# Optimization experiments

Measured on AMD Instinct MI355X. Metric: run time of the kernel, lower is better.

The kernel has to match this reference:

```python
import jax, jax.numpy as jnp
import numpy as np

N_EXPERTS = 64
TOPK = 4
DIM = 2048
B_T = 8192


def setup_inputs() -> dict:
    key = jax.random.key(0)
    k1, k2 = jax.random.split(key)
    x = jax.random.normal(k1, (B_T, DIM), jnp.float32)
    W = jax.random.normal(k2, (N_EXPERTS, DIM), jnp.float32) * 0.02  # nn.Linear weight (out, in)
    router_bias = jnp.zeros((N_EXPERTS,), jnp.float32)  # registered buffer, init zeros
    return {"x": x, "W": W, "router_bias": router_bias, "token_capacity": 3072}


def _route(x, W, router_bias, token_capacity):
    """Faithful serial greedy capacity-aware routing.

    Replicates the torch nested loop (k-major, token-minor order):
      - per step, pick argmax over the token's (mutated) logits among experts
        with remaining capacity;
      - full experts whose logit exceeds the chosen one get permanently set
        to -inf in that token's logit row (exactly what the inner while-style
        loop does);
      - if no expert has capacity, selected stays -1, weight 0, and the whole
        row becomes -inf (torch sets the top expert to -inf n_experts times).
    """
    logits0 = x @ W.T + router_bias                       # (N, E)
    scores = jax.nn.softmax(logits0, axis=-1)             # (N, E)
    cap = token_capacity // TOPK                          # python int
    remaining0 = jnp.full((N_EXPERTS,), float(cap), jnp.float32)
    N = x.shape[0]
    NEG = jnp.float32(-jnp.inf)

    def step(carry, i):
        logits, remaining = carry
        b = i % N                                         # token index (k-major order)
        row = logits[b]                                   # (E,)
        masked = jnp.where(remaining > 0, row, NEG)
        chosen = jnp.argmax(masked)
        ok = remaining[chosen] > 0                        # False only if all experts full
        sel = jnp.where(ok, chosen, -1).astype(jnp.int32)
        w = jnp.where(ok, scores[b, chosen], jnp.float32(0.0))
        full = remaining <= 0
        cval = row[chosen]
        # full experts 'above' the chosen one were visited and zapped to -inf
        new_row = jnp.where(ok,
                            jnp.where(full & (row > cval), NEG, row),
                            jnp.full_like(row, NEG))
        logits = logits.at[b].set(new_row)
        remaining = remaining.at[chosen].add(jnp.where(ok, jnp.float32(-1.0), jnp.float32(0.0)))
        return (logits, remaining), (sel, w)

    (_, _), (sel_f, w_f) = jax.lax.scan(step, (logits0, remaining0),
                                        jnp.arange(TOPK * N))
    selected = sel_f.reshape(TOPK, N).T                   # (N, TOPK)
    weights = w_f.reshape(TOPK, N).T                      # (N, TOPK)
    weights = weights / (weights.sum(axis=-1, keepdims=True) + 1e-8)
    return selected, weights


def reference(x, W, router_bias, token_capacity):
    return _route(x, W, router_bias, token_capacity)
```

## Files before the change

kernel.cpp:

```cpp
#include <hip/hip_runtime.h>
#include <math.h>

#define N_TOK 8192
#define DIM   2048
#define NE    64
#define TOPK  4
#define THETA 2e-3f
#define TPB2  16
#define NBLK  (N_TOK / TPB2)
#define RSTR  260

typedef short bf16x8 __attribute__((ext_vector_type(8)));
typedef float f32x4  __attribute__((ext_vector_type(4)));

#define AS1 __attribute__((address_space(1)))
#define AS3 __attribute__((address_space(3)))

#define OFF_LOGITS 0
#define OFF_MAXV   (OFF_LOGITS + N_TOK * NE)
#define OFF_DENOM  (OFF_MAXV + N_TOK)
#define OFF_W1     (OFF_DENOM + N_TOK)
#define OFF_C1     (OFF_W1 + N_TOK)
#define OFF_NFLAG  (OFF_C1 + N_TOK)
#define OFF_FLAGL  (OFF_NFLAG + 64)
#define OFF_WH     (OFF_FLAGL + N_TOK)
#define OFF_WL     (OFF_WH + NE * DIM / 2)
#define OFF_WT     (OFF_WL + NE * DIM / 2)
#define OFF_WTMP   (OFF_WT + NE * DIM)

__device__ inline void cvt2(float a, float b, unsigned& hi, unsigned& lo) {
    const unsigned ua = __float_as_uint(a), ub = __float_as_uint(b);
    hi = __builtin_amdgcn_perm(ub, ua, 0x07060302u);
    const float ra = a - __uint_as_float(ua & 0xFFFF0000u);
    const float rb = b - __uint_as_float(ub & 0xFFFF0000u);
    lo = __builtin_amdgcn_perm(__float_as_uint(rb), __float_as_uint(ra), 0x07060302u);
}

union FragU { unsigned u[4]; bf16x8 v; uint4 q; };

__device__ inline void make_frags(const float4& p, const float4& q,
                                  bf16x8& hi, bf16x8& lo) {
    FragU H, L;
    cvt2(p.x, p.y, H.u[0], L.u[0]);
    cvt2(p.z, p.w, H.u[1], L.u[1]);
    cvt2(q.x, q.y, H.u[2], L.u[2]);
    cvt2(q.z, q.w, H.u[3], L.u[3]);
    hi = H.v; lo = L.v;
}

__global__ __launch_bounds__(256)
void k_wc(const float* __restrict__ W, unsigned short* __restrict__ wh2,
          unsigned short* __restrict__ wl2, float* __restrict__ wt,
          int* __restrict__ nflag) {
    const int t = blockIdx.x * 256 + threadIdx.x;
    if (t == 0) nflag[0] = 0;
    const int l  = t & 63;
    const int grp = t >> 6;
    const int nt = grp & 3;
    const int kc = grp >> 2;
    const int e  = nt * 16 + (l & 15);
    const int k0 = kc * 32 + (l >> 4) * 8;

    const float4 p = *reinterpret_cast<const float4*>(W + (size_t)e * DIM + k0);
    const float4 q = *reinterpret_cast<const float4*>(W + (size_t)e * DIM + k0 + 4);
    FragU H, L;
    cvt2(p.x, p.y, H.u[0], L.u[0]);
    cvt2(p.z, p.w, H.u[1], L.u[1]);
    cvt2(q.x, q.y, H.u[2], L.u[2]);
    cvt2(q.z, q.w, H.u[3], L.u[3]);
    const size_t off = (size_t)grp * 512 + l * 8;
    *reinterpret_cast<uint4*>(wh2 + off) = H.q;
    *reinterpret_cast<uint4*>(wl2 + off) = L.q;

    wt[(size_t)(k0 + 0) * NE + e] = p.x;
    wt[(size_t)(k0 + 1) * NE + e] = p.y;
    wt[(size_t)(k0 + 2) * NE + e] = p.z;
    wt[(size_t)(k0 + 3) * NE + e] = p.w;
    wt[(size_t)(k0 + 4) * NE + e] = q.x;
    wt[(size_t)(k0 + 5) * NE + e] = q.y;
    wt[(size_t)(k0 + 6) * NE + e] = q.z;
    wt[(size_t)(k0 + 7) * NE + e] = q.w;
}

__global__ __launch_bounds__(512, 4)
void k_main(const float* __restrict__ x, const unsigned short* __restrict__ wh2,
            const unsigned short* __restrict__ wl2, const float* __restrict__ bias,
            float* __restrict__ logits, float* __restrict__ maxv,
            float* __restrict__ denomv, float* __restrict__ w1f,
            int* __restrict__ c1, int* __restrict__ nflag, int* __restrict__ flagl) {
    __shared__ __align__(16) float xs[2][TPB2 * RSTR];
    __shared__ float red[8][TPB2][68];
    __shared__ float lbuf[TPB2][68];

    const int tid = threadIdx.x;
    const int w   = tid >> 6;
    const int l   = tid & 63;
    const int t0  = blockIdx.x * TPB2;
    const int m   = l & 15;
    const int g   = l >> 4;

    const float* xrow0 = x + (size_t)(t0 + 2 * w) * DIM + l * 4;
    const float* xrow1 = x + (size_t)(t0 + 2 * w + 1) * DIM + l * 4;
    AS3 float* lds0 = (AS3 float*)&xs[0][(2 * w) * RSTR];
    AS3 float* lds1 = (AS3 float*)&xs[0][(2 * w + 1) * RSTR];
    const int xs1off = TPB2 * RSTR;

    const unsigned short* bh = wh2 + (size_t)w * 2048 + l * 8;
    const unsigned short* bl = wl2 + (size_t)w * 2048 + l * 8;

    f32x4 accA[4], accB[4];
    #pragma unroll
    for (int nt = 0; nt < 4; ++nt)
        #pragma unroll
        for (int r = 0; r < 4; ++r) { accA[nt][r] = 0.0f; accB[nt][r] = 0.0f; }

    __builtin_amdgcn_global_load_lds((const AS1 void*)xrow0, (AS3 void*)lds0, 16, 0, 0);
    __builtin_amdgcn_global_load_lds((const AS1 void*)xrow1, (AS3 void*)lds1, 16, 0, 0);
    uint4 BH[2][4], BL[2][4];
    #pragma unroll
    for (int nt = 0; nt < 4; ++nt) {
        BH[0][nt] = *reinterpret_cast<const uint4*>(bh + nt * 512);
        BL[0][nt] = *reinterpret_cast<const uint4*>(bl + nt * 512);
    }
    __syncthreads();

    const int aoff = m * RSTR + w * 32 + g * 8;

    #pragma unroll
    for (int win = 0; win < 8; ++win) {
        const int cur = win & 1, nxt = cur ^ 1;
        if (win < 7) {
            __builtin_amdgcn_global_load_lds(
                (const AS1 void*)(xrow0 + (win + 1) * 256),
                (AS3 void*)(lds0 + nxt * xs1off), 16, 0, 0);
            __builtin_amdgcn_global_load_lds(
                (const AS1 void*)(xrow1 + (win + 1) * 256),
                (AS3 void*)(lds1 + nxt * xs1off), 16, 0, 0);
            #pragma unroll
            for (int nt = 0; nt < 4; ++nt) {
                BH[nxt][nt] = *reinterpret_cast<const uint4*>(
                    bh + (size_t)(win + 1) * 16384 + nt * 512);
                BL[nxt][nt] = *reinterpret_cast<const uint4*>(
                    bl + (size_t)(win + 1) * 16384 + nt * 512);
            }
        }

        const float4 p = *reinterpret_cast<const float4*>(&xs[0][cur * xs1off + aoff]);
        const float4 q = *reinterpret_cast<const float4*>(&xs[0][cur * xs1off + aoff + 4]);
        bf16x8 ah, al;
        make_frags(p, q, ah, al);

        #pragma unroll
        for (int nt = 0; nt < 4; ++nt) {
            FragU b; b.q = BH[cur][nt];
            accA[nt] = __builtin_amdgcn_mfma_f32_16x16x32_bf16(ah, b.v, accA[nt], 0, 0, 0);
            accB[nt] = __builtin_amdgcn_mfma_f32_16x16x32_bf16(al, b.v, accB[nt], 0, 0, 0);
        }
        #pragma unroll
        for (int nt = 0; nt < 4; ++nt) {
            FragU b; b.q = BL[cur][nt];
            accB[nt] = __builtin_amdgcn_mfma_f32_16x16x32_bf16(ah, b.v, accB[nt], 0, 0, 0);
        }
        __syncthreads();
    }

    #pragma unroll
    for (int nt = 0; nt < 4; ++nt)
        #pragma unroll
        for (int r = 0; r < 4; ++r)
            red[w][g * 4 + r][nt * 16 + m] = accA[nt][r] + accB[nt][r];
    __syncthreads();

    for (int e2 = tid; e2 < TPB2 * NE; e2 += 512) {
        const int t = e2 >> 6, e = e2 & 63;
        float s = red[0][t][e];
        #pragma unroll
        for (int ww = 1; ww < 8; ++ww) s += red[ww][t][e];
        s += bias[e];
        logits[(size_t)(t0 + t) * NE + e] = s;
        lbuf[t][e] = s;
    }
    __syncthreads();

    #pragma unroll
    for (int tt = 0; tt < 2; ++tt) {
        const int t = w * 2 + tt;
        const float lv = lbuf[t][l];
        float v1 = lv; int i1 = l; float v2 = -INFINITY;
        #pragma unroll
        for (int off = 32; off; off >>= 1) {
            const float ov1 = __shfl_xor(v1, off);
            const int   oi1 = __shfl_xor(i1, off);
            const float ov2 = __shfl_xor(v2, off);
            if (ov1 > v1 || (ov1 == v1 && oi1 < i1)) {
                v2 = fmaxf(v1, ov2); v1 = ov1; i1 = oi1;
            } else {
                v2 = fmaxf(v2, ov1);
            }
        }
        float s = expf(lv - v1);
        #pragma unroll
        for (int off = 32; off; off >>= 1) s += __shfl_xor(s, off);
        if (l == 0) {
            const int row = t0 + t;
            maxv[row]   = v1;
            denomv[row] = s;
            c1[row]     = i1;
            w1f[row]    = 1.0f / s;
            if (v1 - v2 < THETA) {
                const int ix = atomicAdd(nflag, 1);
                flagl[ix] = row;
            }
        }
    }
}

__global__ __launch_bounds__(256)
void k_exact(const int* __restrict__ nflag, const int* __restrict__ flagl,
             const float* __restrict__ x, const float* __restrict__ wt,
             const float* __restrict__ bias, float* __restrict__ logits,
             float* __restrict__ maxv, float* __restrict__ denomv,
             float* __restrict__ w1f, int* __restrict__ c1) {
    __shared__ float part[4][68];
    const int n   = nflag[0];
    const int tid = threadIdx.x;
    const int w   = tid >> 6, l = tid & 63;
    for (int i = blockIdx.x; i < n; i += 64) {
        const int t = flagl[i];
        const float* xr = x + (size_t)t * DIM + w * 512;
        const float* wb = wt + (size_t)(w * 512) * NE + l;
        float a = 0.0f;
        for (int k = 0; k < 512; k += 4) {
            const float4 xv = *reinterpret_cast<const float4*>(xr + k);
            a = fmaf(xv.x, wb[(size_t)(k + 0) * NE], a);
            a = fmaf(xv.y, wb[(size_t)(k + 1) * NE], a);
            a = fmaf(xv.z, wb[(size_t)(k + 2) * NE], a);
            a = fmaf(xv.w, wb[(size_t)(k + 3) * NE], a);
        }
        part[w][l] = a;
        __syncthreads();
        if (w == 0) {
            float lg = bias[l];
            #pragma unroll
            for (int s = 0; s < 4; ++s) lg += part[s][l];
            logits[(size_t)t * NE + l] = lg;
            float v = lg; int idx = l;
            #pragma unroll
            for (int off = 32; off; off >>= 1) {
                const float ov = __shfl_xor(v, off);
                const int   oi = __shfl_xor(idx, off);
                if (ov > v || (ov == v && oi < idx)) { v = ov; idx = oi; }
            }
            float p = expf(lg - v);
            #pragma unroll
            for (int off = 32; off; off >>= 1) p += __shfl_xor(p, off);
            if (l == 0) {
                maxv[t]   = v;
                denomv[t] = p;
                c1[t]     = idx;
                w1f[t]    = 1.0f / p;
            }
        }
        __syncthreads();
    }
}

__global__ __launch_bounds__(256)
void k_decide(const int* __restrict__ c1, const float* __restrict__ w1,
              const float* __restrict__ logits, const float* __restrict__ maxv,
              const float* __restrict__ denomv, const int* __restrict__ tc,
              float* __restrict__ out, float* __restrict__ wtmp) {
    __shared__ int hist[NE];
    __shared__ int flagS;
    const int tid = threadIdx.x;
    if (tid < NE) hist[tid] = 0;
    __syncthreads();
    for (int i = tid; i < N_TOK; i += 256) atomicAdd(&hist[c1[i]], 1);
    __syncthreads();
    const int cap = tc[0] / TOPK;
    if (tid < NE) {
        const bool bad = (TOPK * hist[tid] > cap);
        const unsigned long long mm = __ballot(bad);
        if (tid == 0) flagS = (mm == 0ull) ? 1 : 0;
    }
    __syncthreads();

    if (flagS) {
        const int b = blockIdx.x * 256 + tid;
        const float se = (float)c1[b];
        const float wv = w1[b];
        const float wn = wv / (4.0f * wv + 1e-8f);
        *reinterpret_cast<float4*>(out + (size_t)b * 4) = make_float4(se, se, se, se);
        *reinterpret_cast<float4*>(out + (size_t)N_TOK * TOPK + (size_t)b * 4) =
            make_float4(wn, wn, wn, wn);
        return;
    }

    if (blockIdx.x != 0) return;
    if (tid < 64) {
        const int e = tid;
        int rem = cap;
        for (int k = 0; k < TOPK; ++k) {
            for (int b = 0; b < N_TOK; ++b) {
                const float lg = logits[(size_t)b * NE + e];
                float v = (rem > 0) ? lg : -INFINITY;
                int idx = e;
                #pragma unroll
                for (int off = 32; off; off >>= 1) {
                    const float ov = __shfl_xor(v, off);
                    const int   oi = __shfl_xor(idx, off);
                    if (ov > v || (ov == v && oi < idx)) { v = ov; idx = oi; }
                }
                const bool ok = (v != -INFINITY);
                if (ok && e == idx) rem -= 1;
                const float lc = __shfl(lg, idx);
                if (e == 0) {
                    out[(size_t)b * TOPK + k]  = ok ? (float)idx : -1.0f;
                    wtmp[(size_t)b * TOPK + k] = ok ? expf(lc - maxv[b]) / denomv[b] : 0.0f;
                }
            }
        }
    }
    __syncthreads();
    for (int b = tid; b < N_TOK; b += 256) {
        const float w0 = wtmp[b * 4 + 0], w1_ = wtmp[b * 4 + 1];
        const float w2 = wtmp[b * 4 + 2], w3 = wtmp[b * 4 + 3];
        const float s = ((w0 + w1_) + w2) + w3 + 1e-8f;
        out[N_TOK * TOPK + b * 4 + 0] = w0 / s;
        out[N_TOK * TOPK + b * 4 + 1] = w1_ / s;
        out[N_TOK * TOPK + b * 4 + 2] = w2 / s;
        out[N_TOK * TOPK + b * 4 + 3] = w3 / s;
    }
}

extern "C" void kernel_launch(void* const* d_in, const int* in_sizes, int n_in,
                              void* d_out, int out_size, void* d_ws, size_t ws_size,
                              hipStream_t stream) {
    const float* x    = (const float*)d_in[0];
    const float* W    = (const float*)d_in[1];
    const float* bias = (const float*)d_in[2];
    const int*   tc   = (const int*)d_in[3];

    float* ws       = (float*)d_ws;
    float* logits   = ws + OFF_LOGITS;
    float* maxv     = ws + OFF_MAXV;
    float* denomv   = ws + OFF_DENOM;
    float* w1f      = ws + OFF_W1;
    int*   c1       = (int*)(ws + OFF_C1);
    int*   nflag    = (int*)(ws + OFF_NFLAG);
    int*   flagl    = (int*)(ws + OFF_FLAGL);
    unsigned short* wh2 = (unsigned short*)(ws + OFF_WH);
    unsigned short* wl2 = (unsigned short*)(ws + OFF_WL);
    float* wt       = ws + OFF_WT;
    float* wtmp     = ws + OFF_WTMP;
    float* out      = (float*)d_out;

    k_wc<<<NE * DIM / 8 / 256, 256, 0, stream>>>(W, wh2, wl2, wt, nflag);
    k_main<<<NBLK, 512, 0, stream>>>(x, wh2, wl2, bias, logits, maxv, denomv,
                                     w1f, c1, nflag, flagl);
    k_exact<<<64, 256, 0, stream>>>(nflag, flagl, x, wt, bias, logits,
                                    maxv, denomv, w1f, c1);
    k_decide<<<N_TOK / 256, 256, 0, stream>>>(c1, w1f, logits, maxv, denomv,
                                              tc, out, wtmp);
}
```

Before: 132.4 us.

## Split router GEMM over K into two blocks and combine in separate kernel

The logits GEMM is split along the 2048-wide reduction dimension into two halves via a second grid dimension. Each block writes its partial sums to a workspace buffer, and a new combine kernel adds the partials and bias, then computes the max, second max, softmax denominator and near-tie flags. This doubles the block count (1024 blocks) for better occupancy and latency hiding, at the cost of an extra kernel launch and an extra round trip of partial logits through global memory.

```diff
diff --git a/kernel.cpp b/kernel.cpp
--- a/kernel.cpp
+++ b/kernel.cpp
@@ -8,6 +8,8 @@
 #define THETA 2e-3f
 #define TPB2  16
 #define NBLK  (N_TOK / TPB2)
+#define KSP   2
+#define KPERB (DIM / KSP)
 #define RSTR  260
 
 typedef short bf16x8 __attribute__((ext_vector_type(8)));
@@ -17,7 +19,8 @@
 #define AS3 __attribute__((address_space(3)))
 
 #define OFF_LOGITS 0
-#define OFF_MAXV   (OFF_LOGITS + N_TOK * NE)
+#define OFF_PACC   (OFF_LOGITS + N_TOK * NE)
+#define OFF_MAXV   (OFF_PACC + KSP * N_TOK * NE)
 #define OFF_DENOM  (OFF_MAXV + N_TOK)
 #define OFF_W1     (OFF_DENOM + N_TOK)
 #define OFF_C1     (OFF_W1 + N_TOK)
@@ -84,29 +87,27 @@
 
 __global__ __launch_bounds__(512, 4)
 void k_main(const float* __restrict__ x, const unsigned short* __restrict__ wh2,
-            const unsigned short* __restrict__ wl2, const float* __restrict__ bias,
-            float* __restrict__ logits, float* __restrict__ maxv,
-            float* __restrict__ denomv, float* __restrict__ w1f,
-            int* __restrict__ c1, int* __restrict__ nflag, int* __restrict__ flagl) {
+            const unsigned short* __restrict__ wl2, float* __restrict__ pacc) {
     __shared__ __align__(16) float xs[2][TPB2 * RSTR];
     __shared__ float red[8][TPB2][68];
-    __shared__ float lbuf[TPB2][68];
 
     const int tid = threadIdx.x;
     const int w   = tid >> 6;
     const int l   = tid & 63;
     const int t0  = blockIdx.x * TPB2;
+    const int ks  = blockIdx.y;
+    const int kb  = ks * KPERB;
     const int m   = l & 15;
     const int g   = l >> 4;
 
-    const float* xrow0 = x + (size_t)(t0 + 2 * w) * DIM + l * 4;
-    const float* xrow1 = x + (size_t)(t0 + 2 * w + 1) * DIM + l * 4;
+    const float* xrow0 = x + (size_t)(t0 + 2 * w) * DIM + kb + l * 4;
+    const float* xrow1 = x + (size_t)(t0 + 2 * w + 1) * DIM + kb + l * 4;
     AS3 float* lds0 = (AS3 float*)&xs[0][(2 * w) * RSTR];
     AS3 float* lds1 = (AS3 float*)&xs[0][(2 * w + 1) * RSTR];
     const int xs1off = TPB2 * RSTR;
 
-    const unsigned short* bh = wh2 + (size_t)w * 2048 + l * 8;
-    const unsigned short* bl = wl2 + (size_t)w * 2048 + l * 8;
+    const unsigned short* bh = wh2 + (size_t)(ks * 32 + w) * 2048 + l * 8;
+    const unsigned short* bl = wl2 + (size_t)(ks * 32 + w) * 2048 + l * 8;
 
     f32x4 accA[4], accB[4];
     #pragma unroll
@@ -127,9 +128,9 @@
     const int aoff = m * RSTR + w * 32 + g * 8;
 
     #pragma unroll
-    for (int win = 0; win < 8; ++win) {
+    for (int win = 0; win < 4; ++win) {
         const int cur = win & 1, nxt = cur ^ 1;
-        if (win < 7) {
+        if (win < 3) {
             __builtin_amdgcn_global_load_lds(
                 (const AS1 void*)(xrow0 + (win + 1) * 256),
                 (AS3 void*)(lds0 + nxt * xs1off), 16, 0, 0);
@@ -176,41 +177,46 @@
         float s = red[0][t][e];
         #pragma unroll
         for (int ww = 1; ww < 8; ++ww) s += red[ww][t][e];
-        s += bias[e];
-        logits[(size_t)(t0 + t) * NE + e] = s;
-        lbuf[t][e] = s;
-    }
-    __syncthreads();
-
-    #pragma unroll
-    for (int tt = 0; tt < 2; ++tt) {
-        const int t = w * 2 + tt;
-        const float lv = lbuf[t][l];
-        float v1 = lv; int i1 = l; float v2 = -INFINITY;
-        #pragma unroll
-        for (int off = 32; off; off >>= 1) {
-            const float ov1 = __shfl_xor(v1, off);
-            const int   oi1 = __shfl_xor(i1, off);
-            const float ov2 = __shfl_xor(v2, off);
-            if (ov1 > v1 || (ov1 == v1 && oi1 < i1)) {
-                v2 = fmaxf(v1, ov2); v1 = ov1; i1 = oi1;
-            } else {
-                v2 = fmaxf(v2, ov1);
-            }
-        }
-        float s = expf(lv - v1);
-        #pragma unroll
-        for (int off = 32; off; off >>= 1) s += __shfl_xor(s, off);
-        if (l == 0) {
-            const int row = t0 + t;
-            maxv[row]   = v1;
-            denomv[row] = s;
-            c1[row]     = i1;
-            w1f[row]    = 1.0f / s;
-            if (v1 - v2 < THETA) {
-                const int ix = atomicAdd(nflag, 1);
-                flagl[ix] = row;
-            }
+        pacc[((size_t)ks * N_TOK + t0 + t) * NE + e] = s;
+    }
+}
+
+__global__ __launch_bounds__(256)
+void k_comb(const float* __restrict__ pacc, const float* __restrict__ bias,
+            float* __restrict__ logits, float* __restrict__ maxv,
+            float* __restrict__ denomv, float* __restrict__ w1f,
+            int* __restrict__ c1, int* __restrict__ nflag,
+            int* __restrict__ flagl) {
+    const int row = blockIdx.x * 4 + (threadIdx.x >> 6);
+    const int l   = threadIdx.x & 63;
+    const float lg = pacc[(size_t)row * NE + l]
+                   + pacc[((size_t)N_TOK + row) * NE + l] + bias[l];
+    logits[(size_t)row * NE + l] = lg;
+
+    float v1 = lg; int i1 = l; float v2 = -INFINITY;
+    #pragma unroll
+    for (int off = 32; off; off >>= 1) {
+        const float ov1 = __shfl_xor(v1, off);
+        const int   oi1 = __shfl_xor(i1, off);
+        const float ov2 = __shfl_xor(v2, off);
+        if (ov1 > v1 || (ov1 == v1 && oi1 < i1)) {
+            v2 = fmaxf(v1, ov2); v1 = ov1; i1 = oi1;
+        } else {
+            v2 = fmaxf(v2, ov1);
+        }
+    }
+    float s = expf(lg - v1);
+    #pragma unroll
+    for (int off = 32; off; off >>= 1) s += __shfl_xor(s, off);
+
+    if (l == 0) {
+        maxv[row]   = v1;
+        denomv[row] = s;
+        c1[row]     = i1;
+        w1f[row]    = 1.0f / s;
+        if (v1 - v2 < THETA) {
+            const int ix = atomicAdd(nflag, 1);
+            flagl[ix] = row;
         }
     }
 }
@@ -343,6 +349,7 @@
 
     float* ws       = (float*)d_ws;
     float* logits   = ws + OFF_LOGITS;
+    float* pacc     = ws + OFF_PACC;
     float* maxv     = ws + OFF_MAXV;
     float* denomv   = ws + OFF_DENOM;
     float* w1f      = ws + OFF_W1;
@@ -356,8 +363,10 @@
     float* out      = (float*)d_out;
 
     k_wc<<<NE * DIM / 8 / 256, 256, 0, stream>>>(W, wh2, wl2, wt, nflag);
-    k_main<<<NBLK, 512, 0, stream>>>(x, wh2, wl2, bias, logits, maxv, denomv,
-                                     w1f, c1, nflag, flagl);
+    dim3 g(NBLK, KSP);
+    k_main<<<g, 512, 0, stream>>>(x, wh2, wl2, pacc);
+    k_comb<<<N_TOK / 4, 256, 0, stream>>>(pacc, bias, logits, maxv, denomv,
+                                          w1f, c1, nflag, flagl);
     k_exact<<<64, 256, 0, stream>>>(nflag, flagl, x, wt, bias, logits,
                                     maxv, denomv, w1f, c1);
     k_decide<<<N_TOK / 256, 256, 0, stream>>>(c1, w1f, logits, maxv, denomv,
```

Result: no change. 133.6 us (+0.9%).
